# Performance work log

Hardware: AMD Instinct MI355X
Metric: run time of the kernel (lower is better)

## Reference

```python
import jax, jax.numpy as jnp
import numpy as np

WH, WW = 7, 7
NUM_HEADS = 8

def _relative_position_index(Wh, Ww):
    coords = np.stack(np.meshgrid(np.arange(Wh), np.arange(Ww), indexing='ij'))  # (2, Wh, Ww)
    cf = coords.reshape(2, -1)                       # (2, N)
    rc = cf[:, :, None] - cf[:, None, :]             # (2, N, N)
    rc = rc.transpose(1, 2, 0).astype(np.int64)      # (N, N, 2)
    rc[..., 0] += Wh - 1
    rc[..., 1] += Ww - 1
    rc[..., 0] *= 2 * Ww - 1
    return rc.sum(-1)                                # (N, N)

_REL_IDX = jnp.asarray(_relative_position_index(WH, WW))


def setup_inputs() -> dict:
    key = jax.random.key(0)
    ks = jax.random.split(key, 9)
    B_, N, C = 2048, 49, 256
    nW = 64
    return {
        'x': jax.random.normal(ks[0], (B_, N, C), jnp.float32),
        'mask': jax.random.normal(ks[1], (nW, N, N), jnp.float32),
        'sal_fg_attn_mask': jax.random.normal(ks[2], (B_, N, N), jnp.float32),
        'sal_bg_attn_mask': jax.random.normal(ks[3], (B_, N, N), jnp.float32),
        'qkv_w': jax.random.normal(ks[4], (3 * C, C), jnp.float32) * 0.02,
        'qkv_b': jax.random.normal(ks[5], (3 * C,), jnp.float32) * 0.02,
        'proj_w': jax.random.normal(ks[6], (C, C), jnp.float32) * 0.02,
        'proj_b': jax.random.normal(ks[7], (C,), jnp.float32) * 0.02,
        'rel_pos_bias_table': jax.random.normal(ks[8], ((2 * WH - 1) * (2 * WW - 1), NUM_HEADS), jnp.float32) * 0.02,
    }


def reference(x, mask, sal_fg_attn_mask, sal_bg_attn_mask, qkv_w, qkv_b, proj_w, proj_b, rel_pos_bias_table):
    B_, N, C = x.shape
    H = NUM_HEADS
    hd = C // H
    scale = hd ** -0.5

    qkv = x @ qkv_w.T + qkv_b                        # (B_, N, 3C)
    qkv = qkv.reshape(B_, N, 3, H, hd).transpose(2, 0, 3, 1, 4)  # (3, B_, H, N, hd)
    q, k, v = qkv[0] * scale, qkv[1], qkv[2]

    attn = jnp.einsum('bhqd,bhkd->bhqk', q, k)       # (B_, H, N, N)
    bias = rel_pos_bias_table[_REL_IDX]              # (N, N, H)
    attn = attn + bias.transpose(2, 0, 1)[None]      # broadcast over B_

    attn_fg = attn + sal_fg_attn_mask[:, None]
    attn_bg = attn + sal_bg_attn_mask[:, None]

    nW = mask.shape[0]
    m = mask[None, :, None]                          # (1, nW, 1, N, N)

    def masked_softmax(a):
        a = a.reshape(B_ // nW, nW, H, N, N) + m
        return jax.nn.softmax(a.reshape(B_, H, N, N), axis=-1)

    attn = masked_softmax(attn)
    attn_fg = masked_softmax(attn_fg)
    attn_bg = masked_softmax(attn_bg)

    def av(a):
        return jnp.einsum('bhqk,bhkd->bqhd', a, v).reshape(B_, N, C)

    out = av(attn) + av(attn_fg) - av(attn_bg)
    return out @ proj_w.T + proj_b
```

## Files before the change

kernel.cpp:

```cpp
#include <hip/hip_runtime.h>
#include <hip/hip_bf16.h>
#include <math.h>


#define B_TOT   2048
#define NTOK    49
#define CDIM    256
#define NHEAD   8
#define HDIM    32
#define MROWS   (B_TOT * NTOK)
#define QKV_N   (3 * CDIM)

#define LOG2E 1.4426950408889634f

#if __has_builtin(__builtin_amdgcn_exp2f)
#define EXP2(x) __builtin_amdgcn_exp2f(x)
#else
#define EXP2(x) __expf((x) * 0.6931471805599453f)
#endif

typedef __attribute__((ext_vector_type(8))) short short8;
typedef __attribute__((ext_vector_type(4))) float floatx4;

typedef unsigned int u32_g __attribute__((address_space(1)));
typedef unsigned int u32_l __attribute__((address_space(3)));

__device__ __forceinline__ void gld_lds16(const void* g, void* l) {
    __builtin_amdgcn_global_load_lds((const u32_g*)g, (u32_l*)l, 16, 0, 0);
}

__device__ __forceinline__ void cast8(const float* __restrict__ in,
                                      __hip_bfloat16* __restrict__ out, int i) {
    const float4* p = (const float4*)in + (size_t)i * 2;
    float4 a = p[0], b = p[1];
    __hip_bfloat16 r[8];
    r[0] = __float2bfloat16(a.x); r[1] = __float2bfloat16(a.y);
    r[2] = __float2bfloat16(a.z); r[3] = __float2bfloat16(a.w);
    r[4] = __float2bfloat16(b.x); r[5] = __float2bfloat16(b.y);
    r[6] = __float2bfloat16(b.z); r[7] = __float2bfloat16(b.w);
    *(uint4*)(out + (size_t)i * 8) = *(const uint4*)r;
}

__device__ __forceinline__ void exp4(const float* __restrict__ in,
                                     float* __restrict__ out, int i) {
    float4 a = ((const float4*)in)[i];
    float4 r;
    r.x = EXP2(a.x * LOG2E); r.y = EXP2(a.y * LOG2E);
    r.z = EXP2(a.z * LOG2E); r.w = EXP2(a.w * LOG2E);
    ((float4*)out)[i] = r;
}

__global__ __launch_bounds__(256) void pre_kernel(
    const float* __restrict__ x,
    const float* __restrict__ qkv_w,
    const float* __restrict__ proj_w,
    const float* __restrict__ wmask,
    const float* __restrict__ table,
    const float* __restrict__ fg,
    const float* __restrict__ bg,
    __hip_bfloat16* __restrict__ xb,
    __hip_bfloat16* __restrict__ qwb,
    __hip_bfloat16* __restrict__ pwb,
    float* __restrict__ wmp,
    float* __restrict__ Fgp,
    float* __restrict__ Bgp)
{
    const int bid = blockIdx.x;
    const int t = threadIdx.x;
    if (bid < 12544) {
        cast8(x, xb, bid * 256 + t);
    } else if (bid < 12640) {
        cast8(qkv_w, qwb, (bid - 12544) * 256 + t);
    } else if (bid < 12672) {
        cast8(proj_w, pwb, (bid - 12640) * 256 + t);
    } else if (bid < 20864) {
        const int idx = (bid - 12672) * 256 + t;
        const int col = idx & 63, row = (idx >> 6) & 63;
        const int h = (idx >> 12) & 7, win = idx >> 15;
        float v = -1e30f;
        if (row < 49 && col < 49) {
            const int qi = row / 7, qj = row % 7;
            const int ki = col / 7, kj = col % 7;
            const int ti = (qi - ki + 6) * 13 + (qj - kj + 6);
            v = (wmask[win * 2401 + row * 49 + col] + table[ti * 8 + h]) * LOG2E;
        }
        wmp[idx] = v;
    } else if (bid < 25666) {
        exp4(fg, Fgp, (bid - 20864) * 256 + t);
    } else {
        exp4(bg, Bgp, (bid - 25666) * 256 + t);
    }
}

template<int NDIM, bool OUT_BF16>
__global__ __launch_bounds__(256) void gemm_mfma(
    const __hip_bfloat16* __restrict__ A,
    const __hip_bfloat16* __restrict__ W,
    const float* __restrict__ bias,
    void* __restrict__ Yv)
{
    const int K = 256;
    __shared__ short As[128 * 64];
    __shared__ short Bs[128 * 64];
    const int t = threadIdx.x;
    const int lane = t & 63, w = t >> 6;
    const int wr = w >> 1, wc = w & 1;
    const int q = lane >> 4, l15 = lane & 15;

    constexpr int NBX = NDIM / 128;
    constexpr int NWG = NBX * (MROWS / 128);
    int bid = blockIdx.y * NBX + blockIdx.x;
    bid = (bid & 7) * (NWG >> 3) + (bid >> 3);
    const int m0 = (bid / NBX) * 128, n0 = (bid % NBX) * 128;

    const int srow = t >> 3, skb = t & 7;
    const int gkb = skb ^ (srow & 7);
    const __hip_bfloat16* Ag = A + (size_t)(m0 + srow) * K + gkb * 8;
    const __hip_bfloat16* Wg = W + (size_t)(n0 + srow) * K + gkb * 8;

    floatx4 acc[4][4] = {};
    const int swz = l15 & 7;

    for (int k0 = 0; k0 < K; k0 += 64) {
        __syncthreads();
        #pragma unroll
        for (int i = 0; i < 4; i++) {
            gld_lds16(Ag + (size_t)(i * 32) * K + k0, &As[i * 2048 + w * 512]);
            gld_lds16(Wg + (size_t)(i * 32) * K + k0, &Bs[i * 2048 + w * 512]);
        }
        __syncthreads();
        #pragma unroll
        for (int kk = 0; kk < 2; kk++) {
            const int kbs = ((kk << 2) + q) ^ swz;
            short8 af[4], bf[4];
            #pragma unroll
            for (int i = 0; i < 4; i++) {
                af[i] = *(const short8*)&As[(wr * 64 + i * 16 + l15) * 64 + kbs * 8];
                bf[i] = *(const short8*)&Bs[(wc * 64 + i * 16 + l15) * 64 + kbs * 8];
            }
            #pragma unroll
            for (int i = 0; i < 4; i++)
                #pragma unroll
                for (int j = 0; j < 4; j++)
                    acc[i][j] = __builtin_amdgcn_mfma_f32_16x16x32_bf16(
                        af[i], bf[j], acc[i][j], 0, 0, 0);
        }
    }

    #pragma unroll
    for (int j = 0; j < 4; j++) {
        const int n = n0 + wc * 64 + j * 16 + l15;
        const float bv = bias[n];
        #pragma unroll
        for (int i = 0; i < 4; i++) {
            #pragma unroll
            for (int r = 0; r < 4; r++) {
                const int m = m0 + wr * 64 + i * 16 + q * 4 + r;
                const float val = acc[i][j][r] + bv;
                if (OUT_BF16)
                    ((__hip_bfloat16*)Yv)[(size_t)m * NDIM + n] = __float2bfloat16(val);
                else
                    ((float*)Yv)[(size_t)m * NDIM + n] = val;
            }
        }
    }
}

__global__ __launch_bounds__(256, 6) void attn_kernel(
    const __hip_bfloat16* __restrict__ Y,
    const float* __restrict__ wmp,
    const float* __restrict__ Fgp,
    const float* __restrict__ Bgp,
    __hip_bfloat16* __restrict__ O)
{
    __shared__ __hip_bfloat16 sQ[64 * 40];
    __shared__ __hip_bfloat16 sK[64 * 40];
    __shared__ __hip_bfloat16 sVt[32 * 72];
    __shared__ __hip_bfloat16 sP[64 * 72];

    const int blk = blockIdx.x;
    const int b = (blk >> 6) * 8 + (blk & 7);
    const int h = (blk >> 3) & 7;
    const int t = threadIdx.x;
    const int w = t >> 6, lane = t & 63;
    const int quad = lane >> 4, l15 = lane & 15;
    const float SC = 0.17677669529663687f * LOG2E;

    const float* wmb = wmp + (((size_t)(b & 63) * 8 + h) << 12);
    const float* fgb = Fgp + (size_t)b * (NTOK * NTOK);
    const float* bgb = Bgp + (size_t)b * (NTOK * NTOK);
    float mwm[16], mfg[16], mbg[16];
    #pragma unroll
    for (int r = 0; r < 4; r++) {
        const int row = w * 16 + quad * 4 + r;
        const int rc49 = min(row, 48) * 49;
        const float* pw = wmb + row * 64 + l15;
        const float* pf = fgb + rc49 + l15;
        const float* pb = bgb + rc49 + l15;
        mwm[r * 4 + 0] = pw[0];  mwm[r * 4 + 1] = pw[16];
        mwm[r * 4 + 2] = pw[32]; mwm[r * 4 + 3] = pw[48];
        mfg[r * 4 + 0] = pf[0];  mfg[r * 4 + 1] = pf[16];
        mfg[r * 4 + 2] = pf[32]; mfg[r * 4 + 3] = fgb[rc49 + 48];
        mbg[r * 4 + 0] = pb[0];  mbg[r * 4 + 1] = pb[16];
        mbg[r * 4 + 2] = pb[32]; mbg[r * 4 + 3] = bgb[rc49 + 48];
    }
    const __hip_bfloat16* Yb = Y + (size_t)b * NTOK * QKV_N + h * HDIM;
    if (t < 196) {
        const int n = t >> 2, c = t & 3;
        uint4 qv = *(const uint4*)(Yb + (size_t)n * QKV_N + c * 8);
        uint4 kv = *(const uint4*)(Yb + (size_t)n * QKV_N + 256 + c * 8);
        uint4 vv = *(const uint4*)(Yb + (size_t)n * QKV_N + 512 + c * 8);
        *(uint4*)(sQ + n * 40 + c * 8) = qv;
        *(uint4*)(sK + n * 40 + c * 8) = kv;
        const __hip_bfloat16* vp = (const __hip_bfloat16*)&vv;
        #pragma unroll
        for (int j = 0; j < 8; j++)
            sVt[(c * 8 + j) * 72 + n] = vp[j];
    }
    {
        unsigned int* pK = (unsigned int*)sK;
        #pragma unroll
        for (int i = 980 + t; i < 1280; i += 256) pK[i] = 0u;
    }
    {
        const __hip_bfloat16 z = __float2bfloat16(0.f);
        #pragma unroll
        for (int it = 0; it < 2; it++) {
            const int idx = t + it * 256;
            const int d = idx >> 4, c = 49 + (idx & 15);
            sVt[d * 72 + c] = z;
        }
    }
    __syncthreads();

    floatx4 acc[4];
    {
        short8 af = *(const short8*)(sQ + (w * 16 + l15) * 40 + quad * 8);
        #pragma unroll
        for (int nt = 0; nt < 4; nt++) {
            short8 bf = *(const short8*)(sK + (nt * 16 + l15) * 40 + quad * 8);
            floatx4 z = {};
            acc[nt] = __builtin_amdgcn_mfma_f32_16x16x32_bf16(af, bf, z, 0, 0, 0);
        }
    }

    float e0[16];
    #pragma unroll
    for (int r = 0; r < 4; r++)
        #pragma unroll
        for (int nt = 0; nt < 4; nt++)
            e0[r * 4 + nt] = EXP2(fmaf(acc[nt][r], SC, mwm[r * 4 + nt]));
    #pragma unroll
    for (int i = 0; i < 16; i++) mfg[i] *= e0[i];
    #pragma unroll
    for (int i = 0; i < 16; i++) mbg[i] *= e0[i];

    float s0[4], sf[4], sb[4];
    #pragma unroll
    for (int r = 0; r < 4; r++) {
        s0[r] = (e0[r * 4] + e0[r * 4 + 1]) + (e0[r * 4 + 2] + e0[r * 4 + 3]);
        sf[r] = (mfg[r * 4] + mfg[r * 4 + 1]) + (mfg[r * 4 + 2] + mfg[r * 4 + 3]);
        sb[r] = (mbg[r * 4] + mbg[r * 4 + 1]) + (mbg[r * 4 + 2] + mbg[r * 4 + 3]);
    }
    #pragma unroll
    for (int st = 1; st < 16; st <<= 1)
        #pragma unroll
        for (int r = 0; r < 4; r++) {
            s0[r] += __shfl_xor(s0[r], st);
            sf[r] += __shfl_xor(sf[r], st);
            sb[r] += __shfl_xor(sb[r], st);
        }

    float pc[16];
    #pragma unroll
    for (int r = 0; r < 4; r++) {
        const float r0 = __builtin_amdgcn_rcpf(s0[r]);
        const float rf = __builtin_amdgcn_rcpf(sf[r]);
        const float rb = -__builtin_amdgcn_rcpf(sb[r]);
        #pragma unroll
        for (int nt = 0; nt < 4; nt++) {
            const int i = r * 4 + nt;
            pc[i] = fmaf(mbg[i], rb, fmaf(mfg[i], rf, e0[i] * r0));
        }
    }

    #pragma unroll
    for (int r = 0; r < 4; r++) {
        const int row = w * 16 + quad * 4 + r;
        #pragma unroll
        for (int nt = 0; nt < 4; nt++)
            sP[row * 72 + nt * 16 + l15] = __float2bfloat16(pc[r * 4 + nt]);
    }
    __syncthreads();

    floatx4 o0 = {}, o1 = {};
    {
        short8 a0  = *(const short8*)(sP + (w * 16 + l15) * 72 + quad * 8);
        short8 a1  = *(const short8*)(sP + (w * 16 + l15) * 72 + 32 + quad * 8);
        short8 b00 = *(const short8*)(sVt + l15 * 72 + quad * 8);
        short8 b01 = *(const short8*)(sVt + l15 * 72 + 32 + quad * 8);
        short8 b10 = *(const short8*)(sVt + (16 + l15) * 72 + quad * 8);
        short8 b11 = *(const short8*)(sVt + (16 + l15) * 72 + 32 + quad * 8);
        o0 = __builtin_amdgcn_mfma_f32_16x16x32_bf16(a0, b00, o0, 0, 0, 0);
        o0 = __builtin_amdgcn_mfma_f32_16x16x32_bf16(a1, b01, o0, 0, 0, 0);
        o1 = __builtin_amdgcn_mfma_f32_16x16x32_bf16(a0, b10, o1, 0, 0, 0);
        o1 = __builtin_amdgcn_mfma_f32_16x16x32_bf16(a1, b11, o1, 0, 0, 0);
    }
    __hip_bfloat16* Ob = O + (size_t)b * NTOK * CDIM + h * HDIM;
    #pragma unroll
    for (int r = 0; r < 4; r++) {
        const int m = w * 16 + quad * 4 + r;
        if (m < NTOK) {
            Ob[(size_t)m * CDIM + l15]      = __float2bfloat16(o0[r]);
            Ob[(size_t)m * CDIM + 16 + l15] = __float2bfloat16(o1[r]);
        }
    }
}

extern "C" void kernel_launch(void* const* d_in, const int* in_sizes, int n_in,
                              void* d_out, int out_size, void* d_ws, size_t ws_size,
                              hipStream_t stream) {
    const float* x      = (const float*)d_in[0];
    const float* mask   = (const float*)d_in[1];
    const float* fg     = (const float*)d_in[2];
    const float* bg     = (const float*)d_in[3];
    const float* qkv_w  = (const float*)d_in[4];
    const float* qkv_b  = (const float*)d_in[5];
    const float* proj_w = (const float*)d_in[6];
    const float* proj_b = (const float*)d_in[7];
    const float* table  = (const float*)d_in[8];
    float* out = (float*)d_out;

    char* ws = (char*)d_ws;
    __hip_bfloat16* xb  = (__hip_bfloat16*)(ws);
    __hip_bfloat16* Ybf = (__hip_bfloat16*)(ws + 51380224);
    float* wmp = (float*)(ws + 205520896);
    float* Fgp = (float*)(ws + 213909504);
    float* Bgp = (float*)(ws + 233578496);
    __hip_bfloat16* qwb = (__hip_bfloat16*)(ws + 256901120);
    __hip_bfloat16* pwb = (__hip_bfloat16*)(ws + 257294336);
    __hip_bfloat16* Obf = xb;

    dim3 blk(256);
    pre_kernel<<<dim3(30468), blk, 0, stream>>>(
        x, qkv_w, proj_w, mask, table, fg, bg, xb, qwb, pwb, wmp, Fgp, Bgp);
    gemm_mfma<QKV_N, true><<<dim3(QKV_N / 128, MROWS / 128), blk, 0, stream>>>(xb, qwb, qkv_b, Ybf);
    attn_kernel<<<dim3(B_TOT * NHEAD), blk, 0, stream>>>(Ybf, wmp, Fgp, Bgp, Obf);
    gemm_mfma<CDIM, false><<<dim3(CDIM / 128, MROWS / 128), blk, 0, stream>>>(Obf, pwb, proj_b, out);
}
```

Before: 411.1 us.

## Split QKV-attention-proj pipeline into batch chunks to keep intermediates cache-resident

The x cast now runs per chunk, and the four stages (cast, QKV GEMM, attention, output projection) run over 8 batch chunks in sequence instead of once over the whole batch. The bf16 QKV and attention outputs for a chunk should then still sit in the last-level cache when the next stage reads them, which cuts HBM round trips. The GEMM's XCD block remap is generalised to handle grid sizes that are not multiples of 8. In exchange there are many more kernel launches, and each launch is smaller, so tail underutilisation costs more.

```diff
diff --git a/kernel.cpp b/kernel.cpp
--- a/kernel.cpp
+++ b/kernel.cpp
@@ -10,6 +10,9 @@
 #define HDIM    32
 #define MROWS   (B_TOT * NTOK)
 #define QKV_N   (3 * CDIM)
+#define NCHUNK  8
+#define B_CH    (B_TOT / NCHUNK)
+#define MR_CH   (B_CH * NTOK)
 
 #define LOG2E 1.4426950408889634f
 
@@ -50,15 +53,13 @@
     ((float4*)out)[i] = r;
 }
 
-__global__ __launch_bounds__(256) void pre_kernel(
-    const float* __restrict__ x,
+__global__ __launch_bounds__(256) void pre_masks(
     const float* __restrict__ qkv_w,
     const float* __restrict__ proj_w,
     const float* __restrict__ wmask,
     const float* __restrict__ table,
     const float* __restrict__ fg,
     const float* __restrict__ bg,
-    __hip_bfloat16* __restrict__ xb,
     __hip_bfloat16* __restrict__ qwb,
     __hip_bfloat16* __restrict__ pwb,
     float* __restrict__ wmp,
@@ -67,14 +68,12 @@
 {
     const int bid = blockIdx.x;
     const int t = threadIdx.x;
-    if (bid < 12544) {
-        cast8(x, xb, bid * 256 + t);
-    } else if (bid < 12640) {
-        cast8(qkv_w, qwb, (bid - 12544) * 256 + t);
-    } else if (bid < 12672) {
-        cast8(proj_w, pwb, (bid - 12640) * 256 + t);
-    } else if (bid < 20864) {
-        const int idx = (bid - 12672) * 256 + t;
+    if (bid < 96) {
+        cast8(qkv_w, qwb, bid * 256 + t);
+    } else if (bid < 128) {
+        cast8(proj_w, pwb, (bid - 96) * 256 + t);
+    } else if (bid < 8320) {
+        const int idx = (bid - 128) * 256 + t;
         const int col = idx & 63, row = (idx >> 6) & 63;
         const int h = (idx >> 12) & 7, win = idx >> 15;
         float v = -1e30f;
@@ -85,11 +84,17 @@
             v = (wmask[win * 2401 + row * 49 + col] + table[ti * 8 + h]) * LOG2E;
         }
         wmp[idx] = v;
-    } else if (bid < 25666) {
-        exp4(fg, Fgp, (bid - 20864) * 256 + t);
+    } else if (bid < 13122) {
+        exp4(fg, Fgp, (bid - 8320) * 256 + t);
     } else {
-        exp4(bg, Bgp, (bid - 25666) * 256 + t);
-    }
+        exp4(bg, Bgp, (bid - 13122) * 256 + t);
+    }
+}
+
+__global__ __launch_bounds__(256) void cast_x(
+    const float* __restrict__ in, __hip_bfloat16* __restrict__ out)
+{
+    cast8(in, out, blockIdx.x * 256 + threadIdx.x);
 }
 
 template<int NDIM, bool OUT_BF16>
@@ -108,9 +113,11 @@
     const int q = lane >> 4, l15 = lane & 15;
 
     constexpr int NBX = NDIM / 128;
-    constexpr int NWG = NBX * (MROWS / 128);
-    int bid = blockIdx.y * NBX + blockIdx.x;
-    bid = (bid & 7) * (NWG >> 3) + (bid >> 3);
+    const int nwg = NBX * (int)gridDim.y;
+    const int orig = (int)blockIdx.y * NBX + (int)blockIdx.x;
+    const int xcd = orig & 7, rest = orig >> 3;
+    const int qq = nwg >> 3, rr = nwg & 7;
+    const int bid = (xcd < rr ? xcd * (qq + 1) : rr * (qq + 1) + (xcd - rr) * qq) + rest;
     const int m0 = (bid / NBX) * 128, n0 = (bid % NBX) * 128;
 
     const int srow = t >> 3, skb = t & 7;
@@ -171,7 +178,8 @@
     const float* __restrict__ wmp,
     const float* __restrict__ Fgp,
     const float* __restrict__ Bgp,
-    __hip_bfloat16* __restrict__ O)
+    __hip_bfloat16* __restrict__ O,
+    int b_base)
 {
     __shared__ __hip_bfloat16 sQ[64 * 40];
     __shared__ __hip_bfloat16 sK[64 * 40];
@@ -179,7 +187,7 @@
     __shared__ __hip_bfloat16 sP[64 * 72];
 
     const int blk = blockIdx.x;
-    const int b = (blk >> 6) * 8 + (blk & 7);
+    const int b = b_base + (blk >> 6) * 8 + (blk & 7);
     const int h = (blk >> 3) & 7;
     const int t = threadIdx.x;
     const int w = t >> 6, lane = t & 63;
@@ -342,9 +350,23 @@
     __hip_bfloat16* Obf = xb;
 
     dim3 blk(256);
-    pre_kernel<<<dim3(30468), blk, 0, stream>>>(
-        x, qkv_w, proj_w, mask, table, fg, bg, xb, qwb, pwb, wmp, Fgp, Bgp);
-    gemm_mfma<QKV_N, true><<<dim3(QKV_N / 128, MROWS / 128), blk, 0, stream>>>(xb, qwb, qkv_b, Ybf);
-    attn_kernel<<<dim3(B_TOT * NHEAD), blk, 0, stream>>>(Ybf, wmp, Fgp, Bgp, Obf);
-    gemm_mfma<CDIM, false><<<dim3(CDIM / 128, MROWS / 128), blk, 0, stream>>>(Obf, pwb, proj_b, out);
-}
+    pre_masks<<<dim3(17924), blk, 0, stream>>>(
+        qkv_w, proj_w, mask, table, fg, bg, qwb, pwb, wmp, Fgp, Bgp);
+
+    for (int c = 0; c < NCHUNK; c++) {
+        const size_t ro = (size_t)c * MR_CH;
+        const float* xc = x + ro * CDIM;
+        __hip_bfloat16* xbc = xb + ro * CDIM;
+        __hip_bfloat16* Yc  = Ybf + ro * QKV_N;
+        __hip_bfloat16* Oc  = Obf + ro * CDIM;
+        float* outc = out + ro * CDIM;
+
+        cast_x<<<dim3(MR_CH * CDIM / 8 / 256), blk, 0, stream>>>(xc, xbc);
+        gemm_mfma<QKV_N, true><<<dim3(QKV_N / 128, MR_CH / 128), blk, 0, stream>>>(
+            xbc, qwb, qkv_b, Yc);
+        attn_kernel<<<dim3(B_CH * NHEAD), blk, 0, stream>>>(
+            Ybf, wmp, Fgp, Bgp, Obf, c * B_CH);
+        gemm_mfma<CDIM, false><<<dim3(CDIM / 128, MR_CH / 128), blk, 0, stream>>>(
+            Oc, pwb, proj_b, outc);
+    }
+}
```

After: 484.5 us. 1.18x slower.
